# Performance work log

Hardware: AMD Instinct MI355X
Metric: run time of the kernel (lower is better)

The kernel has to match this reference:

```python
import jax, jax.numpy as jnp
import numpy as np

N_NODES = 50000


def setup_inputs() -> dict:
    key = jax.random.key(0)
    ks = jax.random.split(key, 9)
    x = jax.random.normal(ks[0], (N_NODES, 32), dtype=jnp.float32)
    pos = jax.random.normal(ks[1], (N_NODES, 3), dtype=jnp.float32)
    edge_index = jax.random.randint(ks[2], (2, 1600000), 0, N_NODES, dtype=jnp.int64)
    W1 = jax.random.normal(ks[3], (35, 64), dtype=jnp.float32) * 0.1
    b1 = jnp.zeros((64,), dtype=jnp.float32)
    W2 = jax.random.normal(ks[4], (64, 64), dtype=jnp.float32) * 0.1
    b2 = jnp.zeros((64,), dtype=jnp.float32)
    Wg = jax.random.normal(ks[5], (64, 128), dtype=jnp.float32) * 0.1
    bg = jnp.zeros((128,), dtype=jnp.float32)
    return {"x": x, "pos": pos, "edge_index": edge_index,
            "W1": W1, "b1": b1, "W2": W2, "b2": b2, "Wg": Wg, "bg": bg}


def reference(x, pos, edge_index, W1, b1, W2, b2, Wg, bg):
    N = x.shape[0]
    # add_self_loops=True: append (i, i) edges
    self_idx = jnp.arange(N, dtype=edge_index.dtype)
    src = jnp.concatenate([edge_index[0], self_idx])  # message source j
    dst = jnp.concatenate([edge_index[1], self_idx])  # aggregation target i
    # message: concat(x_j, pos_j - pos_i) -> local_nn (Lin+ReLU x2)
    msg = jnp.concatenate([x[src], pos[src] - pos[dst]], axis=-1)  # [E+N, 35]
    h = jax.nn.relu(msg @ W1 + b1)  # [E+N, 64]
    h = jax.nn.relu(h @ W2 + b2)    # [E+N, 64]
    # max aggregation per destination node (self loops guarantee nonempty segments)
    agg = jax.ops.segment_max(h, dst, num_segments=N)  # [N, 64]
    # global_nn: Linear
    return agg @ Wg + bg  # [N, 128]
```

## Files before the change

### kernel.cpp

```cpp
#include <hip/hip_runtime.h>

#define N_NODES 50000
#define N_EDGES 1600000
#define N_TOTAL (N_EDGES + N_NODES)
#define F_IN    32
#define HID     64
#define F_OUT   128
#define G       32
#define NB      1563
#define NBIN    392
#define CAP1_MAX 5120
#define OVF_CAP 16384
#define W1WIN   4096
#define NNODEBLK 196

#define OFF_QBF   0
#define OFF_CUR1  (N_NODES * 32)
#define OFF_OVFC  (OFF_CUR1 + NBIN * 16)
#define OFF_CELLB (OFF_OVFC + 16)
#define OFF_CELLC (OFF_CELLB + NB)
#define OFF_OVF   (OFF_CELLC + NB + 2)
#define OFF_BIN   (OFF_OVF + OVF_CAP)
#define NCLR      (NBIN * 16 + 16)

typedef __attribute__((ext_vector_type(2))) _Float16 h2f;
typedef __attribute__((ext_vector_type(8))) _Float16 half8;
typedef __attribute__((ext_vector_type(4))) float v4f;

__device__ __forceinline__ unsigned f2h2(float a, float b) {
    h2f v;
    v.x = (_Float16)a; v.y = (_Float16)b;
    return __builtin_bit_cast(unsigned, v);
}

__device__ __forceinline__ unsigned hsubmax0(unsigned a, unsigned b) {
    h2f x = __builtin_bit_cast(h2f, a) - __builtin_bit_cast(h2f, b);
    h2f z = {(_Float16)0.f, (_Float16)0.f};
    x = __builtin_elementwise_max(x, z);
    return __builtin_bit_cast(unsigned, x);
}

#define WAVE_FENCE() do { asm volatile("s_waitcnt lgkmcnt(0)" ::: "memory"); \
                          __builtin_amdgcn_sched_barrier(0); } while (0)

__global__ __launch_bounds__(256) void zero_kernel(unsigned* __restrict__ clr)
{
    const int i = blockIdx.x * 256 + threadIdx.x;
    if (i < NCLR) clr[i] = 0u;
}

__global__ __launch_bounds__(1024) void bin_kernel(
    const int* __restrict__ ei, unsigned* __restrict__ cur1,
    unsigned* __restrict__ bin1, unsigned* __restrict__ ovfc,
    unsigned* __restrict__ ovf, int cap1)
{
    __shared__ unsigned stage[W1WIN];
    __shared__ unsigned hist[NBIN], startp[NBIN + 1], gbase[NBIN];
    __shared__ unsigned wpart[16];

    const int t = threadIdx.x;
    const int wbase = blockIdx.x * W1WIN;

    for (int i = t; i < NBIN; i += 1024) hist[i] = 0u;
    __syncthreads();

    unsigned ev[4]; int bv[4]; unsigned rv[4]; bool val[4];
    #pragma unroll
    for (int k = 0; k < 4; ++k) {
        const int idx = wbase + k * 1024 + t;
        val[k] = idx < N_TOTAL;
        if (val[k]) {
            int s, d;
            if (idx < N_EDGES) { s = ei[idx]; d = ei[N_EDGES + idx]; }
            else               { s = d = idx - N_EDGES; }
            ev[k] = ((unsigned)d << 16) | (unsigned)s;
            bv[k] = d >> 7;
            rv[k] = atomicAdd(&hist[bv[k]], 1u);
        }
    }
    __syncthreads();

    unsigned hv = 0;
    if (t < NBIN) hv = hist[t];
    unsigned v = hv;
    #pragma unroll
    for (int o = 1; o < 64; o <<= 1) {
        const unsigned u = __shfl_up(v, o, 64);
        if ((t & 63) >= o) v += u;
    }
    if ((t & 63) == 63) wpart[t >> 6] = v;
    __syncthreads();
    if (t == 0) {
        unsigned r = 0;
        #pragma unroll
        for (int i = 0; i < 16; ++i) { const unsigned c2 = wpart[i]; wpart[i] = r; r += c2; }
        startp[NBIN] = r;
    }
    __syncthreads();
    if (t < NBIN) startp[t] = (v - hv) + wpart[t >> 6];
    if (t < NBIN && hv) gbase[t] = atomicAdd(&cur1[t * 16], hv);
    __syncthreads();

    #pragma unroll
    for (int k = 0; k < 4; ++k)
        if (val[k]) stage[startp[bv[k]] + rv[k]] = ev[k];
    __syncthreads();

    const unsigned total = startp[NBIN];
    for (unsigned i = t; i < total; i += 1024u) {
        const unsigned e = stage[i];
        const unsigned b = e >> 23;
        const unsigned gp = gbase[b] + (i - startp[b]);
        if (gp < (unsigned)cap1) bin1[b * (unsigned)cap1 + gp] = e;
        else {
            const unsigned qo = atomicAdd(ovfc, 1u);
            if (qo < OVF_CAP) ovf[qo] = e;
        }
    }
}

__global__ __launch_bounds__(1024) void refine_pre_kernel(
    unsigned* __restrict__ bin1, const unsigned* __restrict__ cur1,
    unsigned* __restrict__ cellbase, unsigned* __restrict__ cellcnt, int cap1,
    const float* __restrict__ x, const float* __restrict__ pos,
    const float* __restrict__ W1, const float* __restrict__ b1,
    unsigned* __restrict__ qbf)
{
    __shared__ unsigned ebuf[CAP1_MAX];
    __shared__ unsigned ebuf2[CAP1_MAX];
    __shared__ unsigned cnt32[4 * 32];
    __shared__ unsigned startp[5];
    __shared__ unsigned ssum;
    __shared__ float    w1s[35 * HID + HID];

    const int t = threadIdx.x;

    if (blockIdx.x >= NBIN) {
        for (int i = t; i < 35 * HID; i += 1024) w1s[i] = W1[i];
        if (t < HID) w1s[35 * HID + t] = b1[t];
        __syncthreads();

        const int n = (blockIdx.x - NBIN) * 256 + (t >> 2);
        const int sub = t & 3;
        const int lane = t & 63;
        if (n >= N_NODES) return;

        const float4* x4 = (const float4*)(x + (long long)n * F_IN);
        const float4 xa = x4[sub * 2], xb = x4[sub * 2 + 1];
        const float xv[8] = {xa.x, xa.y, xa.z, xa.w, xb.x, xb.y, xb.z, xb.w};

        float acc[16];
        #pragma unroll
        for (int k = 0; k < 16; ++k) acc[k] = w1s[35 * HID + sub * 16 + k];

        #pragma unroll
        for (int c = 0; c < F_IN; ++c) {
            const float xm = __shfl(xv[c & 7], (lane & 60) | (c >> 3), 64);
            #pragma unroll
            for (int k = 0; k < 16; ++k)
                acc[k] = fmaf(xm, w1s[c * HID + sub * 16 + k], acc[k]);
        }
        #pragma unroll
        for (int a = 0; a < 3; ++a) {
            const float pp = pos[n * 3 + a];
            #pragma unroll
            for (int k = 0; k < 16; ++k)
                acc[k] = fmaf(pp, w1s[(F_IN + a) * HID + sub * 16 + k], acc[k]);
        }

        uint4* o4 = (uint4*)(qbf + (unsigned)n * 32u + (unsigned)sub * 8u);
        o4[0] = make_uint4(f2h2(acc[0], acc[1]),  f2h2(acc[2], acc[3]),
                           f2h2(acc[4], acc[5]),  f2h2(acc[6], acc[7]));
        o4[1] = make_uint4(f2h2(acc[8], acc[9]),  f2h2(acc[10], acc[11]),
                           f2h2(acc[12], acc[13]), f2h2(acc[14], acc[15]));
        return;
    }

    const int bb = blockIdx.x;
    const unsigned n1 = min(cur1[bb * 16], (unsigned)cap1);
    const unsigned base1 = (unsigned)bb * (unsigned)cap1;
    const int rep = t & 31, lane = t & 63;

    if (t < 128) cnt32[t] = 0u;
    __syncthreads();

    for (unsigned i = t; i < n1; i += 1024u) {
        const unsigned e = bin1[base1 + i];
        ebuf[i] = e;
        atomicAdd(&cnt32[(((e >> 21) & 3u) << 5) + rep], 1u);
    }
    __syncthreads();

    unsigned ow = 0;
    if (t < 128) ow = cnt32[t];
    unsigned v = ow;
    #pragma unroll
    for (int o = 1; o < 64; o <<= 1) {
        const unsigned u = __shfl_up(v, o, 64);
        if (lane >= o) v += u;
    }
    if (t == 63) ssum = v;
    __syncthreads();
    if (t >= 64 && t < 128) v += ssum;
    if (t < 128) {
        cnt32[t] = v - ow;
        if ((t & 31) == 0) startp[t >> 5] = v - ow;
    }
    if (t == 0) startp[4] = n1;
    __syncthreads();

    if (t < 4) {
        const int cell = bb * 4 + t;
        if (cell < NB) {
            cellbase[cell] = base1 + startp[t];
            cellcnt[cell]  = startp[t + 1] - startp[t];
        }
    }

    for (unsigned i = t; i < n1; i += 1024u) {
        const unsigned e = ebuf[i];
        const unsigned p = atomicAdd(&cnt32[(((e >> 21) & 3u) << 5) + rep], 1u);
        ebuf2[p] = (((e >> 16) & 31u) << 16) | (e & 0xFFFFu);
    }
    __syncthreads();
    for (unsigned i = t; i < n1; i += 1024u) bin1[base1 + i] = ebuf2[i];
}

__global__ __launch_bounds__(256, 4) void gather_kernel(
    const unsigned* __restrict__ qbf,
    const float* __restrict__ pos,
    const unsigned* __restrict__ cellbase,
    const unsigned* __restrict__ cellcnt,
    const unsigned* __restrict__ bkt,
    const unsigned* __restrict__ ovfc, const unsigned* __restrict__ ovf,
    const float* __restrict__ W1p,
    const float* __restrict__ W2, const float* __restrict__ b2,
    const float* __restrict__ Wg, const float* __restrict__ bg,
    float* __restrict__ out)
{
    __shared__ unsigned aggs[(G + 1) * HID];
    __shared__ unsigned rlds[G * 32];
    __shared__ unsigned ast[4][64 * 16];

    const int t = threadIdx.x, lane = t & 63, w = t >> 6;
    const int q = lane >> 4, m15 = lane & 15;
    const int b = blockIdx.x;
    const unsigned cnt  = cellcnt[b];
    const unsigned base = cellbase[b];
    const unsigned no   = min(*ovfc, (unsigned)OVF_CAP);
    const unsigned tot  = cnt + no;

    for (int i = t; i < (G + 1) * HID; i += 256) aggs[i] = 0u;
    for (int i = t; i < G * 32; i += 256) {
        const int dl = i >> 5, k2 = i & 31;
        const int node = b * G + dl;
        float v0 = 0.f, v1 = 0.f;
        if (node < N_NODES) {
            #pragma unroll
            for (int a = 0; a < 3; ++a) {
                const float pp = pos[node * 3 + a];
                v0 = fmaf(pp, W1p[a * HID + 2 * k2], v0);
                v1 = fmaf(pp, W1p[a * HID + 2 * k2 + 1], v1);
            }
        }
        rlds[(dl << 5) + ((((k2 >> 2) ^ (dl & 7)) << 2) | (k2 & 3))] = f2h2(v0, v1);
    }

    half8 bfr[2][2][2];
    #pragma unroll
    for (int h = 0; h < 2; ++h)
        #pragma unroll
        for (int ntl = 0; ntl < 2; ++ntl) {
            const int nn = (2 * h + ntl) * 16 + m15;
            #pragma unroll
            for (int ks = 0; ks < 2; ++ks) {
                half8 vv;
                #pragma unroll
                for (int j = 0; j < 4; ++j) {
                    const int ku = (ks * 4 + q) * 4 + j;
                    vv[2 * j]     = (_Float16)W2[(2 * ku) * HID + nn];
                    vv[2 * j + 1] = (_Float16)W2[(2 * ku + 1) * HID + nn];
                }
                bfr[h][ntl][ks] = vv;
            }
        }
    float b2v[4];
    #pragma unroll
    for (int nt = 0; nt < 4; ++nt) b2v[nt] = b2[nt * 16 + m15];
    __syncthreads();

    unsigned* aw = ast[w];
    const int axw = ((lane >> 1) & 3) << 2;
    const int axr = ((m15 >> 1) & 3) << 2;
    const unsigned nit = (tot + 255u) >> 8;

    #pragma unroll 1
    for (unsigned it = 0; it < nit; ++it) {
        const unsigned off = it * 256u + (unsigned)w * 64u;
        const unsigned f = off + (unsigned)lane;
        int s = 0, dle_lane = G;
        if (f < cnt) {
            const unsigned p2 = bkt[base + f];
            s = (int)(p2 & 0xFFFFu); dle_lane = (int)(p2 >> 16);
        } else if (f < tot) {
            const unsigned p2 = ovf[f - cnt];
            s = (int)(p2 & 0xFFFFu);
            if ((p2 >> 21) == (unsigned)b) dle_lane = (int)((p2 >> 16) & 31u);
        }
        const int dl = (dle_lane < G) ? dle_lane : 0;

        const uint4* qr = (const uint4*)(qbf + (unsigned)s * 32u);
        const int rbase = dl << 5, rx = dl & 7;

        half8 a0[4], a1[4];

        uint4 qva[4];
        #pragma unroll
        for (int i = 0; i < 4; ++i) qva[i] = qr[i];

        uint4 hh0[4];
        #pragma unroll
        for (int j4 = 0; j4 < 4; ++j4) {
            const uint4 r4 = *(const uint4*)(rlds + rbase + ((j4 ^ rx) << 2));
            hh0[j4].x = hsubmax0(qva[j4].x, r4.x);
            hh0[j4].y = hsubmax0(qva[j4].y, r4.y);
            hh0[j4].z = hsubmax0(qva[j4].z, r4.z);
            hh0[j4].w = hsubmax0(qva[j4].w, r4.w);
        }
        uint4 qvb[4];
        #pragma unroll
        for (int i = 0; i < 4; ++i) qvb[i] = qr[i + 4];

        #pragma unroll
        for (int j4 = 0; j4 < 4; ++j4)
            *(uint4*)(aw + (lane << 4) + ((j4 << 2) ^ axw)) = hh0[j4];
        WAVE_FENCE();
        #pragma unroll
        for (int mt = 0; mt < 4; ++mt)
            a0[mt] = *(const half8*)(
                aw + ((mt * 16 + m15) << 4) + ((q << 2) ^ axr));
        WAVE_FENCE();

        #pragma unroll
        for (int j4 = 0; j4 < 4; ++j4) {
            const uint4 r4 = *(const uint4*)(
                rlds + rbase + (((4 + j4) ^ rx) << 2));
            uint4 hh;
            hh.x = hsubmax0(qvb[j4].x, r4.x);
            hh.y = hsubmax0(qvb[j4].y, r4.y);
            hh.z = hsubmax0(qvb[j4].z, r4.z);
            hh.w = hsubmax0(qvb[j4].w, r4.w);
            *(uint4*)(aw + (lane << 4) + ((j4 << 2) ^ axw)) = hh;
        }
        WAVE_FENCE();
        #pragma unroll
        for (int mt = 0; mt < 4; ++mt)
            a1[mt] = *(const half8*)(
                aw + ((mt * 16 + m15) << 4) + ((q << 2) ^ axr));
        WAVE_FENCE();

        #pragma unroll
        for (int h = 0; h < 2; ++h) {
            v4f c[4][2];
            #pragma unroll
            for (int mt = 0; mt < 4; ++mt)
                #pragma unroll
                for (int ntl = 0; ntl < 2; ++ntl) {
                    const float bb2 = b2v[2 * h + ntl];
                    c[mt][ntl] = (v4f){bb2, bb2, bb2, bb2};
                }
            #pragma unroll
            for (int mt = 0; mt < 4; ++mt)
                #pragma unroll
                for (int ntl = 0; ntl < 2; ++ntl) {
                    c[mt][ntl] = __builtin_amdgcn_mfma_f32_16x16x32_f16(
                        a0[mt], bfr[h][ntl][0], c[mt][ntl], 0, 0, 0);
                    c[mt][ntl] = __builtin_amdgcn_mfma_f32_16x16x32_f16(
                        a1[mt], bfr[h][ntl][1], c[mt][ntl], 0, 0, 0);
                }
            #pragma unroll
            for (int mt = 0; mt < 4; ++mt)
                #pragma unroll
                for (int r = 0; r < 4; ++r) {
                    const int er = mt * 16 + q * 4 + r;
                    const int dv = __shfl(dle_lane, er, 64);
                    const int ab = (dv << 6) + m15;
                    #pragma unroll
                    for (int ntl = 0; ntl < 2; ++ntl) {
                        const float hv = fmaxf(c[mt][ntl][r], 0.f);
                        atomicMax(&aggs[ab + (2 * h + ntl) * 16],
                                  __float_as_uint(hv));
                    }
                }
        }
    }

    __syncthreads();
    unsigned* wg16 = &ast[0][0];
    for (int i = t; i < 128 * 32; i += 256) {
        const int nn = i >> 5, ku = i & 31;
        wg16[(nn << 5) + ((((ku >> 2) ^ (nn & 7)) << 2) | (ku & 3))] =
            f2h2(Wg[(2 * ku) * F_OUT + nn], Wg[(2 * ku + 1) * F_OUT + nn]);
    }
    __syncthreads();

    half8 af[2][2];
    #pragma unroll
    for (int mt2 = 0; mt2 < 2; ++mt2)
        #pragma unroll
        for (int ks = 0; ks < 2; ++ks) {
            const unsigned* ap = aggs + (mt2 * 16 + m15) * 64 + ks * 32 + q * 8;
            const uint4 u0 = *(const uint4*)ap;
            const uint4 u1 = *(const uint4*)(ap + 4);
            uint4 pk;
            pk.x = f2h2(__uint_as_float(u0.x), __uint_as_float(u0.y));
            pk.y = f2h2(__uint_as_float(u0.z), __uint_as_float(u0.w));
            pk.z = f2h2(__uint_as_float(u1.x), __uint_as_float(u1.y));
            pk.w = f2h2(__uint_as_float(u1.z), __uint_as_float(u1.w));
            af[mt2][ks] = __builtin_bit_cast(half8, pk);
        }

    #pragma unroll
    for (int ntl = 0; ntl < 2; ++ntl) {
        const int nn = w * 32 + ntl * 16 + m15;
        const float bgv = bg[nn];
        half8 bf[2];
        #pragma unroll
        for (int ks = 0; ks < 2; ++ks)
            bf[ks] = *(const half8*)(
                wg16 + (nn << 5) + ((((ks * 4 + q) ^ (nn & 7)) << 2)));
        #pragma unroll
        for (int mt2 = 0; mt2 < 2; ++mt2) {
            v4f c = (v4f){bgv, bgv, bgv, bgv};
            c = __builtin_amdgcn_mfma_f32_16x16x32_f16(af[mt2][0], bf[0], c, 0, 0, 0);
            c = __builtin_amdgcn_mfma_f32_16x16x32_f16(af[mt2][1], bf[1], c, 0, 0, 0);
            #pragma unroll
            for (int r = 0; r < 4; ++r) {
                const int n = b * G + mt2 * 16 + q * 4 + r;
                if (n < N_NODES) out[(long long)n * F_OUT + nn] = c[r];
            }
        }
    }
}

extern "C" void kernel_launch(void* const* d_in, const int* in_sizes, int n_in,
                              void* d_out, int out_size, void* d_ws, size_t ws_size,
                              hipStream_t stream) {
    const float* x   = (const float*)d_in[0];
    const float* pos = (const float*)d_in[1];
    const int*   ei  = (const int*)d_in[2];
    const float* W1  = (const float*)d_in[3];
    const float* b1  = (const float*)d_in[4];
    const float* W2  = (const float*)d_in[5];
    const float* b2  = (const float*)d_in[6];
    const float* Wg  = (const float*)d_in[7];
    const float* bg  = (const float*)d_in[8];
    float* out = (float*)d_out;

    unsigned* ws    = (unsigned*)d_ws;
    unsigned* qbf   = ws + OFF_QBF;
    unsigned* cur1  = ws + OFF_CUR1;
    unsigned* ovfc  = ws + OFF_OVFC;
    unsigned* cellb = ws + OFF_CELLB;
    unsigned* cellc = ws + OFF_CELLC;
    unsigned* ovf   = ws + OFF_OVF;
    unsigned* bin1  = ws + OFF_BIN;

    long long avail = (long long)(ws_size / 4) - OFF_BIN;
    int cap1 = (int)(avail / NBIN);
    if (cap1 > CAP1_MAX) cap1 = CAP1_MAX;
    if (cap1 < 2048) cap1 = 2048;

    zero_kernel<<<(NCLR + 255) / 256, 256, 0, stream>>>(cur1);
    bin_kernel<<<(N_TOTAL + W1WIN - 1) / W1WIN, 1024, 0, stream>>>(
        ei, cur1, bin1, ovfc, ovf, cap1);
    refine_pre_kernel<<<NBIN + NNODEBLK, 1024, 0, stream>>>(
        bin1, cur1, cellb, cellc, cap1, x, pos, W1, b1, qbf);
    gather_kernel<<<NB, 256, 0, stream>>>(
        qbf, pos, cellb, cellc, bin1, ovfc, ovf,
        W1 + F_IN * HID, W2, b2, Wg, bg, out);
}
```

Baseline: 186.5 us.

## Merge zero, bin and refine kernels into one cooperative persistent kernel

Replaces three separate launches (zero, bin, refine/pre-transform) with a single cooperative kernel of 256 blocks that uses grid-wide syncs between phases and loops over work items persistently. The aim is to remove kernel launch and inter-kernel drain overhead. In exchange, the grid is capped at 256 blocks of 1024 threads, so each block processes several windows or bins serially, and grid.sync adds its own cost. It also relies on the cooperative launch succeeding with this shared-memory footprint.

```diff
diff --git a/kernel.cpp b/kernel.cpp
--- a/kernel.cpp
+++ b/kernel.cpp
@@ -1,4 +1,7 @@
 #include <hip/hip_runtime.h>
+#include <hip/hip_cooperative_groups.h>
+
+namespace cg = cooperative_groups;
 
 #define N_NODES 50000
 #define N_EDGES 1600000
@@ -12,7 +15,9 @@
 #define CAP1_MAX 5120
 #define OVF_CAP 16384
 #define W1WIN   4096
+#define NBINBLK  403
 #define NNODEBLK 196
+#define SORT_BLOCKS 256
 
 #define OFF_QBF   0
 #define OFF_CUR1  (N_NODES * 32)
@@ -43,187 +48,198 @@
 #define WAVE_FENCE() do { asm volatile("s_waitcnt lgkmcnt(0)" ::: "memory"); \
                           __builtin_amdgcn_sched_barrier(0); } while (0)
 
-__global__ __launch_bounds__(256) void zero_kernel(unsigned* __restrict__ clr)
-{
-    const int i = blockIdx.x * 256 + threadIdx.x;
-    if (i < NCLR) clr[i] = 0u;
-}
-
-__global__ __launch_bounds__(1024) void bin_kernel(
-    const int* __restrict__ ei, unsigned* __restrict__ cur1,
-    unsigned* __restrict__ bin1, unsigned* __restrict__ ovfc,
-    unsigned* __restrict__ ovf, int cap1)
-{
-    __shared__ unsigned stage[W1WIN];
-    __shared__ unsigned hist[NBIN], startp[NBIN + 1], gbase[NBIN];
-    __shared__ unsigned wpart[16];
-
-    const int t = threadIdx.x;
-    const int wbase = blockIdx.x * W1WIN;
-
-    for (int i = t; i < NBIN; i += 1024) hist[i] = 0u;
-    __syncthreads();
-
-    unsigned ev[4]; int bv[4]; unsigned rv[4]; bool val[4];
-    #pragma unroll
-    for (int k = 0; k < 4; ++k) {
-        const int idx = wbase + k * 1024 + t;
-        val[k] = idx < N_TOTAL;
-        if (val[k]) {
-            int s, d;
-            if (idx < N_EDGES) { s = ei[idx]; d = ei[N_EDGES + idx]; }
-            else               { s = d = idx - N_EDGES; }
-            ev[k] = ((unsigned)d << 16) | (unsigned)s;
-            bv[k] = d >> 7;
-            rv[k] = atomicAdd(&hist[bv[k]], 1u);
-        }
-    }
-    __syncthreads();
-
-    unsigned hv = 0;
-    if (t < NBIN) hv = hist[t];
-    unsigned v = hv;
-    #pragma unroll
-    for (int o = 1; o < 64; o <<= 1) {
-        const unsigned u = __shfl_up(v, o, 64);
-        if ((t & 63) >= o) v += u;
-    }
-    if ((t & 63) == 63) wpart[t >> 6] = v;
-    __syncthreads();
-    if (t == 0) {
-        unsigned r = 0;
-        #pragma unroll
-        for (int i = 0; i < 16; ++i) { const unsigned c2 = wpart[i]; wpart[i] = r; r += c2; }
-        startp[NBIN] = r;
-    }
-    __syncthreads();
-    if (t < NBIN) startp[t] = (v - hv) + wpart[t >> 6];
-    if (t < NBIN && hv) gbase[t] = atomicAdd(&cur1[t * 16], hv);
-    __syncthreads();
-
-    #pragma unroll
-    for (int k = 0; k < 4; ++k)
-        if (val[k]) stage[startp[bv[k]] + rv[k]] = ev[k];
-    __syncthreads();
-
-    const unsigned total = startp[NBIN];
-    for (unsigned i = t; i < total; i += 1024u) {
-        const unsigned e = stage[i];
-        const unsigned b = e >> 23;
-        const unsigned gp = gbase[b] + (i - startp[b]);
-        if (gp < (unsigned)cap1) bin1[b * (unsigned)cap1 + gp] = e;
-        else {
-            const unsigned qo = atomicAdd(ovfc, 1u);
-            if (qo < OVF_CAP) ovf[qo] = e;
-        }
-    }
-}
-
-__global__ __launch_bounds__(1024) void refine_pre_kernel(
-    unsigned* __restrict__ bin1, const unsigned* __restrict__ cur1,
-    unsigned* __restrict__ cellbase, unsigned* __restrict__ cellcnt, int cap1,
+__global__ __launch_bounds__(1024) void sort_kernel(
+    const int* __restrict__ ei,
+    unsigned* __restrict__ cur1, unsigned* __restrict__ bin1,
+    unsigned* __restrict__ ovfc, unsigned* __restrict__ ovf, int cap1,
+    unsigned* __restrict__ cellbase, unsigned* __restrict__ cellcnt,
     const float* __restrict__ x, const float* __restrict__ pos,
     const float* __restrict__ W1, const float* __restrict__ b1,
     unsigned* __restrict__ qbf)
 {
-    __shared__ unsigned ebuf[CAP1_MAX];
-    __shared__ unsigned ebuf2[CAP1_MAX];
-    __shared__ unsigned cnt32[4 * 32];
-    __shared__ unsigned startp[5];
-    __shared__ unsigned ssum;
-    __shared__ float    w1s[35 * HID + HID];
-
-    const int t = threadIdx.x;
-
-    if (blockIdx.x >= NBIN) {
-        for (int i = t; i < 35 * HID; i += 1024) w1s[i] = W1[i];
-        if (t < HID) w1s[35 * HID + t] = b1[t];
-        __syncthreads();
-
-        const int n = (blockIdx.x - NBIN) * 256 + (t >> 2);
-        const int sub = t & 3;
-        const int lane = t & 63;
-        if (n >= N_NODES) return;
-
-        const float4* x4 = (const float4*)(x + (long long)n * F_IN);
-        const float4 xa = x4[sub * 2], xb = x4[sub * 2 + 1];
-        const float xv[8] = {xa.x, xa.y, xa.z, xa.w, xb.x, xb.y, xb.z, xb.w};
-
-        float acc[16];
-        #pragma unroll
-        for (int k = 0; k < 16; ++k) acc[k] = w1s[35 * HID + sub * 16 + k];
-
-        #pragma unroll
-        for (int c = 0; c < F_IN; ++c) {
-            const float xm = __shfl(xv[c & 7], (lane & 60) | (c >> 3), 64);
-            #pragma unroll
-            for (int k = 0; k < 16; ++k)
-                acc[k] = fmaf(xm, w1s[c * HID + sub * 16 + k], acc[k]);
-        }
-        #pragma unroll
-        for (int a = 0; a < 3; ++a) {
-            const float pp = pos[n * 3 + a];
-            #pragma unroll
-            for (int k = 0; k < 16; ++k)
-                acc[k] = fmaf(pp, w1s[(F_IN + a) * HID + sub * 16 + k], acc[k]);
-        }
-
-        uint4* o4 = (uint4*)(qbf + (unsigned)n * 32u + (unsigned)sub * 8u);
-        o4[0] = make_uint4(f2h2(acc[0], acc[1]),  f2h2(acc[2], acc[3]),
-                           f2h2(acc[4], acc[5]),  f2h2(acc[6], acc[7]));
-        o4[1] = make_uint4(f2h2(acc[8], acc[9]),  f2h2(acc[10], acc[11]),
-                           f2h2(acc[12], acc[13]), f2h2(acc[14], acc[15]));
-        return;
+    cg::grid_group grid = cg::this_grid();
+    __shared__ unsigned shm[10376];
+    const int t = threadIdx.x, lane = t & 63;
+
+    for (int i = blockIdx.x * 1024 + t; i < NCLR; i += SORT_BLOCKS * 1024)
+        cur1[i] = 0u;
+    grid.sync();
+
+    {
+        unsigned* stage  = shm;
+        unsigned* hist   = shm + 4096;
+        unsigned* startp = shm + 4488;
+        unsigned* gbase  = shm + 4881;
+        unsigned* wpart  = shm + 5273;
+
+        for (int win = blockIdx.x; win < NBINBLK; win += SORT_BLOCKS) {
+            const int wbase = win * W1WIN;
+
+            for (int i = t; i < NBIN; i += 1024) hist[i] = 0u;
+            __syncthreads();
+
+            unsigned ev[4]; int bv[4]; unsigned rv[4]; bool val[4];
+            #pragma unroll
+            for (int k = 0; k < 4; ++k) {
+                const int idx = wbase + k * 1024 + t;
+                val[k] = idx < N_TOTAL;
+                if (val[k]) {
+                    int s, d;
+                    if (idx < N_EDGES) { s = ei[idx]; d = ei[N_EDGES + idx]; }
+                    else               { s = d = idx - N_EDGES; }
+                    ev[k] = ((unsigned)d << 16) | (unsigned)s;
+                    bv[k] = d >> 7;
+                    rv[k] = atomicAdd(&hist[bv[k]], 1u);
+                }
+            }
+            __syncthreads();
+
+            unsigned hv = 0;
+            if (t < NBIN) hv = hist[t];
+            unsigned v = hv;
+            #pragma unroll
+            for (int o = 1; o < 64; o <<= 1) {
+                const unsigned u = __shfl_up(v, o, 64);
+                if (lane >= o) v += u;
+            }
+            if (lane == 63) wpart[t >> 6] = v;
+            __syncthreads();
+            if (t == 0) {
+                unsigned r = 0;
+                #pragma unroll
+                for (int i = 0; i < 16; ++i) {
+                    const unsigned c2 = wpart[i]; wpart[i] = r; r += c2;
+                }
+                startp[NBIN] = r;
+            }
+            __syncthreads();
+            if (t < NBIN) startp[t] = (v - hv) + wpart[t >> 6];
+            if (t < NBIN && hv) gbase[t] = atomicAdd(&cur1[t * 16], hv);
+            __syncthreads();
+
+            #pragma unroll
+            for (int k = 0; k < 4; ++k)
+                if (val[k]) stage[startp[bv[k]] + rv[k]] = ev[k];
+            __syncthreads();
+
+            const unsigned total = startp[NBIN];
+            for (unsigned i = t; i < total; i += 1024u) {
+                const unsigned e = stage[i];
+                const unsigned b = e >> 23;
+                const unsigned gp = gbase[b] + (i - startp[b]);
+                if (gp < (unsigned)cap1) bin1[b * (unsigned)cap1 + gp] = e;
+                else {
+                    const unsigned qo = atomicAdd(ovfc, 1u);
+                    if (qo < OVF_CAP) ovf[qo] = e;
+                }
+            }
+            __syncthreads();
+        }
     }
-
-    const int bb = blockIdx.x;
-    const unsigned n1 = min(cur1[bb * 16], (unsigned)cap1);
-    const unsigned base1 = (unsigned)bb * (unsigned)cap1;
-    const int rep = t & 31, lane = t & 63;
-
-    if (t < 128) cnt32[t] = 0u;
-    __syncthreads();
-
-    for (unsigned i = t; i < n1; i += 1024u) {
-        const unsigned e = bin1[base1 + i];
-        ebuf[i] = e;
-        atomicAdd(&cnt32[(((e >> 21) & 3u) << 5) + rep], 1u);
+    grid.sync();
+
+    for (int item = blockIdx.x; item < NBIN + NNODEBLK; item += SORT_BLOCKS) {
+        if (item < NBIN) {
+            unsigned* ebuf   = shm;
+            unsigned* ebuf2  = shm + 5120;
+            unsigned* cnt32  = shm + 10240;
+            unsigned* stp5   = shm + 10368;
+            unsigned* ssum   = shm + 10373;
+
+            const int bb = item;
+            const unsigned n1 = min(cur1[bb * 16], (unsigned)cap1);
+            const unsigned base1 = (unsigned)bb * (unsigned)cap1;
+            const int rep = t & 31;
+
+            if (t < 128) cnt32[t] = 0u;
+            __syncthreads();
+
+            for (unsigned i = t; i < n1; i += 1024u) {
+                const unsigned e = bin1[base1 + i];
+                ebuf[i] = e;
+                atomicAdd(&cnt32[(((e >> 21) & 3u) << 5) + rep], 1u);
+            }
+            __syncthreads();
+
+            unsigned ow = 0;
+            if (t < 128) ow = cnt32[t];
+            unsigned v = ow;
+            #pragma unroll
+            for (int o = 1; o < 64; o <<= 1) {
+                const unsigned u = __shfl_up(v, o, 64);
+                if (lane >= o) v += u;
+            }
+            if (t == 63) *ssum = v;
+            __syncthreads();
+            if (t >= 64 && t < 128) v += *ssum;
+            if (t < 128) {
+                cnt32[t] = v - ow;
+                if ((t & 31) == 0) stp5[t >> 5] = v - ow;
+            }
+            if (t == 0) stp5[4] = n1;
+            __syncthreads();
+
+            if (t < 4) {
+                const int cell = bb * 4 + t;
+                if (cell < NB) {
+                    cellbase[cell] = base1 + stp5[t];
+                    cellcnt[cell]  = stp5[t + 1] - stp5[t];
+                }
+            }
+
+            for (unsigned i = t; i < n1; i += 1024u) {
+                const unsigned e = ebuf[i];
+                const unsigned p = atomicAdd(&cnt32[(((e >> 21) & 3u) << 5) + rep], 1u);
+                ebuf2[p] = (((e >> 16) & 31u) << 16) | (e & 0xFFFFu);
+            }
+            __syncthreads();
+            for (unsigned i = t; i < n1; i += 1024u)
+                bin1[base1 + i] = ebuf2[i];
+            __syncthreads();
+        } else {
+            float* w1s = (float*)shm;
+            __syncthreads();
+
+            for (int i = t; i < 35 * HID; i += 1024) w1s[i] = W1[i];
+            if (t < HID) w1s[35 * HID + t] = b1[t];
+            __syncthreads();
+
+            const int n = (item - NBIN) * 256 + (t >> 2);
+            const int sub = t & 3;
+            if (n < N_NODES) {
+                const float4* x4 = (const float4*)(x + (long long)n * F_IN);
+                const float4 xa = x4[sub * 2], xb = x4[sub * 2 + 1];
+                const float xv[8] = {xa.x, xa.y, xa.z, xa.w,
+                                     xb.x, xb.y, xb.z, xb.w};
+
+                float acc[16];
+                #pragma unroll
+                for (int k = 0; k < 16; ++k) acc[k] = w1s[35 * HID + sub * 16 + k];
+
+                #pragma unroll
+                for (int c = 0; c < F_IN; ++c) {
+                    const float xm = __shfl(xv[c & 7], (lane & 60) | (c >> 3), 64);
+                    #pragma unroll
+                    for (int k = 0; k < 16; ++k)
+                        acc[k] = fmaf(xm, w1s[c * HID + sub * 16 + k], acc[k]);
+                }
+                #pragma unroll
+                for (int a = 0; a < 3; ++a) {
+                    const float pp = pos[n * 3 + a];
+                    #pragma unroll
+                    for (int k = 0; k < 16; ++k)
+                        acc[k] = fmaf(pp, w1s[(F_IN + a) * HID + sub * 16 + k], acc[k]);
+                }
+
+                uint4* o4 = (uint4*)(qbf + (unsigned)n * 32u + (unsigned)sub * 8u);
+                o4[0] = make_uint4(f2h2(acc[0], acc[1]),  f2h2(acc[2], acc[3]),
+                                   f2h2(acc[4], acc[5]),  f2h2(acc[6], acc[7]));
+                o4[1] = make_uint4(f2h2(acc[8], acc[9]),  f2h2(acc[10], acc[11]),
+                                   f2h2(acc[12], acc[13]), f2h2(acc[14], acc[15]));
+            }
+            __syncthreads();
+        }
     }
-    __syncthreads();
-
-    unsigned ow = 0;
-    if (t < 128) ow = cnt32[t];
-    unsigned v = ow;
-    #pragma unroll
-    for (int o = 1; o < 64; o <<= 1) {
-        const unsigned u = __shfl_up(v, o, 64);
-        if (lane >= o) v += u;
-    }
-    if (t == 63) ssum = v;
-    __syncthreads();
-    if (t >= 64 && t < 128) v += ssum;
-    if (t < 128) {
-        cnt32[t] = v - ow;
-        if ((t & 31) == 0) startp[t >> 5] = v - ow;
-    }
-    if (t == 0) startp[4] = n1;
-    __syncthreads();
-
-    if (t < 4) {
-        const int cell = bb * 4 + t;
-        if (cell < NB) {
-            cellbase[cell] = base1 + startp[t];
-            cellcnt[cell]  = startp[t + 1] - startp[t];
-        }
-    }
-
-    for (unsigned i = t; i < n1; i += 1024u) {
-        const unsigned e = ebuf[i];
-        const unsigned p = atomicAdd(&cnt32[(((e >> 21) & 3u) << 5) + rep], 1u);
-        ebuf2[p] = (((e >> 16) & 31u) << 16) | (e & 0xFFFFu);
-    }
-    __syncthreads();
-    for (unsigned i = t; i < n1; i += 1024u) bin1[base1 + i] = ebuf2[i];
 }
 
 __global__ __launch_bounds__(256, 4) void gather_kernel(
@@ -471,11 +487,14 @@
     if (cap1 > CAP1_MAX) cap1 = CAP1_MAX;
     if (cap1 < 2048) cap1 = 2048;
 
-    zero_kernel<<<(NCLR + 255) / 256, 256, 0, stream>>>(cur1);
-    bin_kernel<<<(N_TOTAL + W1WIN - 1) / W1WIN, 1024, 0, stream>>>(
-        ei, cur1, bin1, ovfc, ovf, cap1);
-    refine_pre_kernel<<<NBIN + NNODEBLK, 1024, 0, stream>>>(
-        bin1, cur1, cellb, cellc, cap1, x, pos, W1, b1, qbf);
+    void* sort_args[] = {
+        (void*)&ei, (void*)&cur1, (void*)&bin1, (void*)&ovfc, (void*)&ovf,
+        (void*)&cap1, (void*)&cellb, (void*)&cellc,
+        (void*)&x, (void*)&pos, (void*)&W1, (void*)&b1, (void*)&qbf
+    };
+    hipLaunchCooperativeKernel((const void*)sort_kernel,
+                               dim3(SORT_BLOCKS), dim3(1024),
+                               sort_args, 0, stream);
     gather_kernel<<<NB, 256, 0, stream>>>(
         qbf, pos, cellb, cellc, bin1, ovfc, ovf,
         W1 + F_IN * HID, W2, b2, Wg, bg, out);
```

Measured after the change: 261.8 us. 40.3% more time.

## Software-prefetch next iteration's edge entries and source features; pad aggregation rows

Applied to the files above, without the earlier changes.

The gather loop now loads the next iteration's bucket entry and the first half of the next source node's feature row before the MFMA/atomic phase, so global-memory latency overlaps with compute. The shared aggregation buffer rows are padded from 64 to 68 words, aiming to spread LDS atomicMax traffic across banks. The prefetch costs extra live registers, which could reduce occupancy under the launch bounds.

```diff
diff --git a/kernel.cpp b/kernel.cpp
--- a/kernel.cpp
+++ b/kernel.cpp
@@ -13,6 +13,7 @@
 #define OVF_CAP 16384
 #define W1WIN   4096
 #define NNODEBLK 196
+#define AGS     68
 
 #define OFF_QBF   0
 #define OFF_CUR1  (N_NODES * 32)
@@ -238,7 +239,7 @@
     const float* __restrict__ Wg, const float* __restrict__ bg,
     float* __restrict__ out)
 {
-    __shared__ unsigned aggs[(G + 1) * HID];
+    __shared__ unsigned aggs[(G + 1) * AGS];
     __shared__ unsigned rlds[G * 32];
     __shared__ unsigned ast[4][64 * 16];
 
@@ -250,7 +251,7 @@
     const unsigned no   = min(*ovfc, (unsigned)OVF_CAP);
     const unsigned tot  = cnt + no;
 
-    for (int i = t; i < (G + 1) * HID; i += 256) aggs[i] = 0u;
+    for (int i = t; i < (G + 1) * AGS; i += 256) aggs[i] = 0u;
     for (int i = t; i < G * 32; i += 256) {
         const int dl = i >> 5, k2 = i & 31;
         const int node = b * G + dl;
@@ -294,38 +295,48 @@
     const int axr = ((m15 >> 1) & 3) << 2;
     const unsigned nit = (tot + 255u) >> 8;
 
+    const unsigned f0 = (unsigned)(w * 64 + lane);
+    unsigned pentC = 0u;
+    if (f0 < cnt) pentC = bkt[base + f0];
+    else if (f0 < tot) pentC = ovf[f0 - cnt];
+    uint4 qvaP[4];
+    {
+        const uint4* qr0 = (const uint4*)(qbf + (pentC & 0xFFFFu) * 32u);
+        #pragma unroll
+        for (int i = 0; i < 4; ++i) qvaP[i] = qr0[i];
+    }
+
     #pragma unroll 1
     for (unsigned it = 0; it < nit; ++it) {
         const unsigned off = it * 256u + (unsigned)w * 64u;
         const unsigned f = off + (unsigned)lane;
         int s = 0, dle_lane = G;
         if (f < cnt) {
-            const unsigned p2 = bkt[base + f];
-            s = (int)(p2 & 0xFFFFu); dle_lane = (int)(p2 >> 16);
+            s = (int)(pentC & 0xFFFFu); dle_lane = (int)(pentC >> 16);
         } else if (f < tot) {
-            const unsigned p2 = ovf[f - cnt];
-            s = (int)(p2 & 0xFFFFu);
-            if ((p2 >> 21) == (unsigned)b) dle_lane = (int)((p2 >> 16) & 31u);
+            s = (int)(pentC & 0xFFFFu);
+            if ((pentC >> 21) == (unsigned)b) dle_lane = (int)((pentC >> 16) & 31u);
         }
         const int dl = (dle_lane < G) ? dle_lane : 0;
+
+        const unsigned fN = f + 256u;
+        unsigned pentN = 0u;
+        if (fN < cnt) pentN = bkt[base + fN];
+        else if (fN < tot) pentN = ovf[fN - cnt];
 
         const uint4* qr = (const uint4*)(qbf + (unsigned)s * 32u);
         const int rbase = dl << 5, rx = dl & 7;
 
         half8 a0[4], a1[4];
 
-        uint4 qva[4];
-        #pragma unroll
-        for (int i = 0; i < 4; ++i) qva[i] = qr[i];
-
         uint4 hh0[4];
         #pragma unroll
         for (int j4 = 0; j4 < 4; ++j4) {
             const uint4 r4 = *(const uint4*)(rlds + rbase + ((j4 ^ rx) << 2));
-            hh0[j4].x = hsubmax0(qva[j4].x, r4.x);
-            hh0[j4].y = hsubmax0(qva[j4].y, r4.y);
-            hh0[j4].z = hsubmax0(qva[j4].z, r4.z);
-            hh0[j4].w = hsubmax0(qva[j4].w, r4.w);
+            hh0[j4].x = hsubmax0(qvaP[j4].x, r4.x);
+            hh0[j4].y = hsubmax0(qvaP[j4].y, r4.y);
+            hh0[j4].z = hsubmax0(qvaP[j4].z, r4.z);
+            hh0[j4].w = hsubmax0(qvaP[j4].w, r4.w);
         }
         uint4 qvb[4];
         #pragma unroll
@@ -359,6 +370,12 @@
                 aw + ((mt * 16 + m15) << 4) + ((q << 2) ^ axr));
         WAVE_FENCE();
 
+        {
+            const uint4* qrN = (const uint4*)(qbf + (pentN & 0xFFFFu) * 32u);
+            #pragma unroll
+            for (int i = 0; i < 4; ++i) qvaP[i] = qrN[i];
+        }
+
         #pragma unroll
         for (int h = 0; h < 2; ++h) {
             v4f c[4][2];
@@ -384,7 +401,7 @@
                 for (int r = 0; r < 4; ++r) {
                     const int er = mt * 16 + q * 4 + r;
                     const int dv = __shfl(dle_lane, er, 64);
-                    const int ab = (dv << 6) + m15;
+                    const int ab = dv * AGS + m15;
                     #pragma unroll
                     for (int ntl = 0; ntl < 2; ++ntl) {
                         const float hv = fmaxf(c[mt][ntl][r], 0.f);
@@ -393,6 +410,7 @@
                     }
                 }
         }
+        pentC = pentN;
     }
 
     __syncthreads();
@@ -409,7 +427,7 @@
     for (int mt2 = 0; mt2 < 2; ++mt2)
         #pragma unroll
         for (int ks = 0; ks < 2; ++ks) {
-            const unsigned* ap = aggs + (mt2 * 16 + m15) * 64 + ks * 32 + q * 8;
+            const unsigned* ap = aggs + (mt2 * 16 + m15) * AGS + ks * 32 + q * 8;
             const uint4 u0 = *(const uint4*)ap;
             const uint4 u1 = *(const uint4*)(ap + 4);
             uint4 pk;
```

Measured after the change: 261.2 us. 1.4x slower.
